# Kernel optimization log

Hardware: AMD Instinct MI355X
Metric: run time of the kernel (lower is better)

Reference implementation:

```python
import jax, jax.numpy as jnp
import numpy as np

# Config mirrors cfg['cluster'] and point_cloud_range from init_kwargs
PCR = np.array([-51.2, -51.2, -5.0, 51.2, 51.2, 3.0], dtype=np.float32)
VOXEL_SIZE = 0.2
SIZE_X = 512  # floor((51.2 - (-51.2)) / 0.2)
EPS = 1.5
MIN_SAMPLES = 5
MIN_P_CLUSTER = 20


def _cluster(points):
    """Faithful jax version of Cluster.forward for batch_size == 1.

    voxel_down_sample -> DBSCAN (euclidean, eps, min_samples) on voxel coords
    -> drop clusters with < MIN_P_CLUSTER voxels -> scatter labels back to points.
    """
    N = points.shape[0]
    # --- voxel_down_sample ---
    coords = jnp.floor((points[:, 1:3] - PCR[:2]) / VOXEL_SIZE).astype(jnp.int32)  # (N,2) x,y
    merged = coords[:, 1] * SIZE_X + coords[:, 0]
    # static-size unique: padded entries get fill_value=-1 at the end
    uniq, inv = jnp.unique(merged, size=N, fill_value=-1, return_inverse=True)
    valid = uniq >= 0  # (N,) real voxels
    vox = jnp.stack([uniq % SIZE_X, uniq // SIZE_X], axis=1).astype(jnp.float32)  # (N,2)

    # --- DBSCAN on voxel coords ---
    d2 = jnp.sum((vox[:, None, :] - vox[None, :, :]) ** 2, axis=-1)  # (N,N)
    adj = (d2 <= EPS * EPS) & valid[:, None] & valid[None, :]  # includes self-edge
    core = (jnp.sum(adj, axis=1) >= MIN_SAMPLES) & valid  # sklearn counts self

    BIG = N  # sentinel > any label
    labels0 = jnp.where(core, jnp.arange(N), BIG)
    adj_core = adj & core[None, :]

    def min_core_neighbor(labels):
        return jnp.min(jnp.where(adj_core, labels[None, :], BIG), axis=1)

    def body(carry):
        labels, _ = carry
        new = jnp.where(core, jnp.minimum(labels, min_core_neighbor(labels)), labels)
        return new, jnp.any(new != labels)

    # min-label propagation = connected components over core-core eps graph
    labels, _ = jax.lax.while_loop(lambda c: c[1], body, (labels0, jnp.array(True)))

    # border points attach to a neighboring core cluster; otherwise noise (-1)
    nb = min_core_neighbor(labels)
    raw = jnp.where(core, labels, jnp.where(valid & (nb < BIG), nb, -1))  # root-id or -1

    # relabel root-ids to consecutive 0..k-1 (sklearn numbering by smallest core idx)
    roots = jnp.unique(raw, size=N, fill_value=BIG)  # sorted; BIG padding at end
    pos = jnp.searchsorted(roots, raw)
    dense = pos - (roots[0] == -1).astype(pos.dtype)
    dense = jnp.where(raw >= 0, dense, -1)

    # drop small clusters (by voxel count), keep remaining ids unchanged
    counts = jnp.zeros(N, jnp.int32).at[jnp.where(dense >= 0, dense, 0)].add(
        jnp.where(dense >= 0, 1, 0))
    keep = counts >= MIN_P_CLUSTER
    final = jnp.where((dense >= 0) & keep[jnp.clip(dense, 0, N - 1)], dense, -1)

    # scatter voxel labels back to points (points_inst_idx has points.dtype, like torch)
    pts_inst = final[inv].astype(points.dtype)
    max_num_inst = jnp.maximum(jnp.max(final) + 1, 0)
    return pts_inst, max_num_inst


def setup_inputs() -> dict:
    key = jax.random.key(0)
    N = 8192
    k1, k2, k3, k4, k5, k6, k7 = jax.random.split(key, 7)
    n_blobs = 64
    centers = jax.random.uniform(k1, (n_blobs, 2), minval=-48.0, maxval=48.0)
    assign = jax.random.randint(k2, (N,), 0, n_blobs)
    xy = centers[assign] + jax.random.normal(k3, (N, 2)) * 1.0
    noise = jax.random.uniform(k4, (N,)) < 0.2
    xy = jnp.where(noise[:, None], jax.random.uniform(k5, (N, 2), minval=-51.0, maxval=51.0), xy)
    xy = jnp.clip(xy, -51.0, 51.0)
    z = jax.random.uniform(k6, (N, 1), minval=-3.0, maxval=1.0)
    feat = jax.random.normal(k7, (N, 1))
    points = jnp.concatenate([jnp.zeros((N, 1)), xy, z, feat], axis=1).astype(jnp.float32)
    return {"points": points, "batch_size": 1}


def reference(points, batch_size):
    # voxel_down_sample asserts batch_size == 1; single-batch path.
    return _cluster(points)
```

## Files before the change

kernel.cpp:

```cpp
#include <hip/hip_runtime.h>
#include <stdint.h>


#define GRIDW 512
#define WPR 16
#define NWORDS 8192
#define NCELLS 262144
#define NONE 0xFFFFFFFFu

#define OFF_OCC    0
#define OFF_ROOTBM 8192
#define OFF_CM     16384
#define OFF_LAB    24576
#define OFF_CNT    286720
#define FILL_BYTES (NWORDS * 4)

__device__ __forceinline__ void hsum(uint32_t l, uint32_t c, uint32_t r,
                                     uint32_t& h0, uint32_t& h1) {
  uint32_t Wb = (c << 1) | (l >> 31);
  uint32_t Eb = (c >> 1) | (r << 31);
  h0 = Wb ^ c ^ Eb;
  h1 = (Wb & c) | (Eb & (Wb ^ c));
}

__device__ __forceinline__ uint32_t ge5(uint32_t a0, uint32_t a1, uint32_t b0,
                                        uint32_t b1, uint32_t c0, uint32_t c1) {
  uint32_t u0 = a0 ^ b0, cy = a0 & b0;
  uint32_t t = a1 ^ b1;
  uint32_t u1 = t ^ cy;
  uint32_t u2 = (a1 & b1) | (cy & t);
  uint32_t v0 = u0 ^ c0, k0 = u0 & c0;
  uint32_t t2 = u1 ^ c1;
  uint32_t v1 = t2 ^ k0;
  uint32_t k1 = (u1 & c1) | (k0 & t2);
  uint32_t v2 = u2 ^ k1;
  uint32_t v3 = u2 & k1;
  return v3 | (v2 & (v1 | v0));
}

__device__ __forceinline__ uint32_t aread(uint32_t* p) {
  return __hip_atomic_load(p, __ATOMIC_RELAXED, __HIP_MEMORY_SCOPE_AGENT);
}

__device__ __forceinline__ uint32_t findc(uint32_t* L, uint32_t x) {
  uint32_t r = x, p = aread(&L[r]);
  while (p != r) { r = p; p = aread(&L[r]); }
  while (x > r) {
    uint32_t nx = aread(&L[x]);
    if (nx <= r) break;
    atomicCAS(&L[x], nx, r);
    x = nx;
  }
  return r;
}

__device__ __forceinline__ void unite(uint32_t* L, uint32_t a, uint32_t b) {
  for (;;) {
    a = findc(L, a);
    b = findc(L, b);
    if (a == b) return;
    uint32_t lo = min(a, b), hi = max(a, b);
    if (atomicCAS(&L[hi], hi, lo) == hi) return;
    a = lo; b = hi;
  }
}

__global__ void k_vox(const float* __restrict__ pts, uint32_t* __restrict__ ws,
                      int npts) {
  int i = blockIdx.x * 256 + threadIdx.x;
  if (i >= npts) return;
  float x = pts[i * 5 + 1];
  float y = pts[i * 5 + 2];
  int cx = (int)floorf((x - (-51.2f)) / 0.2f);
  int cy = (int)floorf((y - (-51.2f)) / 0.2f);
  cx = min(max(cx, 0), GRIDW - 1);
  cy = min(max(cy, 0), GRIDW - 1);
  int cell = cy * GRIDW + cx;
  uint32_t old = atomicOr(&ws[OFF_OCC + (cell >> 5)], 1u << (cell & 31));
  if (!((old >> (cell & 31)) & 1)) {
    ws[OFF_LAB + cell] = (uint32_t)cell;
    ws[OFF_CNT + cell] = 0u;
  }
}

__global__ void k_cm(uint32_t* __restrict__ ws) {
  int wi = blockIdx.x * 256 + threadIdx.x;
  const uint32_t* occ = ws + OFF_OCC;
  ws[OFF_ROOTBM + wi] = 0u;
  uint32_t cB = occ[wi];
  int y = wi >> 4, wx = wi & 15;
  uint32_t lB = wx ? occ[wi - 1] : 0u;
  uint32_t rB = (wx < 15) ? occ[wi + 1] : 0u;
  uint32_t cA = 0, lA = 0, rA = 0, cC = 0, lC = 0, rC = 0;
  if (y > 0) { int w = wi - WPR; cA = occ[w]; lA = wx ? occ[w - 1] : 0u; rA = (wx < 15) ? occ[w + 1] : 0u; }
  if (y < GRIDW - 1) { int w = wi + WPR; cC = occ[w]; lC = wx ? occ[w - 1] : 0u; rC = (wx < 15) ? occ[w + 1] : 0u; }
  uint32_t a0, a1, b0, b1, c0, c1;
  hsum(lA, cA, rA, a0, a1); hsum(lB, cB, rB, b0, b1); hsum(lC, cC, rC, c0, c1);
  ws[OFF_CM + wi] = ge5(a0, a1, b0, b1, c0, c1) & cB;
}

__global__ void k_merge(uint32_t* __restrict__ ws) {
  int cell = blockIdx.x * 256 + threadIdx.x;
  const uint32_t* cm = ws + OFF_CM;
  uint32_t* lab = ws + OFF_LAB;
  int wi = cell >> 5, b = cell & 31, wx = wi & 15, y = cell >> 9;
  uint32_t cw0 = cm[wi];
  if (!((cw0 >> b) & 1)) return;
  bool eC = (b < 31) ? (((cw0 >> (b + 1)) & 1) != 0)
                     : ((wx < 15) ? ((cm[wi + 1] & 1u) != 0) : false);
  if (eC) unite(lab, cell, cell + 1);
  if (y < GRIDW - 1) {
    uint32_t cmS = cm[wi + WPR];
    if ((cmS >> b) & 1) unite(lab, cell, cell + GRIDW);
    bool seC = (b < 31) ? (((cmS >> (b + 1)) & 1) != 0)
                        : ((wx < 15) ? ((cm[wi + WPR + 1] & 1u) != 0) : false);
    if (seC) unite(lab, cell, cell + GRIDW + 1);
    bool swC = (b > 0) ? (((cmS >> (b - 1)) & 1) != 0)
                       : ((wx > 0) ? ((cm[wi + WPR - 1] >> 31) != 0) : false);
    if (swC) unite(lab, cell, cell + GRIDW - 1);
  }
}

__global__ void k_cb(uint32_t* __restrict__ ws) {
  int cell = blockIdx.x * 256 + threadIdx.x;
  const uint32_t* occ = ws + OFF_OCC;
  const uint32_t* cm = ws + OFF_CM;
  uint32_t* lab = ws + OFF_LAB;
  uint32_t* cnt = ws + OFF_CNT;
  int wi = cell >> 5, b = cell & 31, wx = wi & 15, y = cell >> 9;
  if (!((occ[wi] >> b) & 1)) return;
  uint32_t cw0 = cm[wi];
  if ((cw0 >> b) & 1) {
    uint32_t root = findc(lab, cell);
    lab[cell] = root;
    if (root == (uint32_t)cell) atomicOr(&ws[OFF_ROOTBM + wi], 1u << b);
    atomicAdd(&cnt[root], 1u);
  } else {
    uint32_t m = NONE;
    bool t;
    t = (b > 0) ? (((cw0 >> (b - 1)) & 1) != 0)
                : ((wx > 0) ? ((cm[wi - 1] >> 31) != 0) : false);
    if (t) m = min(m, findc(lab, cell - 1));
    t = (b < 31) ? (((cw0 >> (b + 1)) & 1) != 0)
                 : ((wx < 15) ? ((cm[wi + 1] & 1u) != 0) : false);
    if (t) m = min(m, findc(lab, cell + 1));
    if (y > 0) {
      uint32_t cmN = cm[wi - WPR];
      if ((cmN >> b) & 1) m = min(m, findc(lab, cell - GRIDW));
      t = (b > 0) ? (((cmN >> (b - 1)) & 1) != 0)
                  : ((wx > 0) ? ((cm[wi - WPR - 1] >> 31) != 0) : false);
      if (t) m = min(m, findc(lab, cell - GRIDW - 1));
      t = (b < 31) ? (((cmN >> (b + 1)) & 1) != 0)
                   : ((wx < 15) ? ((cm[wi - WPR + 1] & 1u) != 0) : false);
      if (t) m = min(m, findc(lab, cell - GRIDW + 1));
    }
    if (y < GRIDW - 1) {
      uint32_t cmS = cm[wi + WPR];
      if ((cmS >> b) & 1) m = min(m, findc(lab, cell + GRIDW));
      t = (b > 0) ? (((cmS >> (b - 1)) & 1) != 0)
                  : ((wx > 0) ? ((cm[wi + WPR - 1] >> 31) != 0) : false);
      if (t) m = min(m, findc(lab, cell + GRIDW - 1));
      t = (b < 31) ? (((cmS >> (b + 1)) & 1) != 0)
                   : ((wx < 15) ? ((cm[wi + WPR + 1] & 1u) != 0) : false);
      if (t) m = min(m, findc(lab, cell + GRIDW + 1));
    }
    lab[cell] = m;
    if (m != NONE) atomicAdd(&cnt[m], 1u);
  }
}

__global__ __launch_bounds__(256) void k_scatter(
    const float* __restrict__ pts, uint32_t* __restrict__ ws,
    float* __restrict__ out, int npts) {
  __shared__ uint32_t rpre_s[NWORDS];
  __shared__ uint32_t keep_s[NWORDS];
  __shared__ uint32_t wsum[4];
  __shared__ int smax;
  int tid = threadIdx.x;
  if (tid == 0) smax = -1;
  int base = tid * 32;
  uint32_t s = 0;
  for (int j = 0; j < 32; j++) s += __popc(ws[OFF_ROOTBM + base + j]);
  int lane = tid & 63, wv = tid >> 6;
  uint32_t inc = s;
  for (int d = 1; d < 64; d <<= 1) { uint32_t t = __shfl_up(inc, d); if (lane >= d) inc += t; }
  if (lane == 63) wsum[wv] = inc;
  __syncthreads();
  uint32_t woff = 0;
  for (int k = 0; k < wv; k++) woff += wsum[k];
  uint32_t excl = woff + inc - s;
  int mx = -1;
  for (int j = 0; j < 32; j++) {
    uint32_t rbw = ws[OFF_ROOTBM + base + j];
    rpre_s[base + j] = excl;
    uint32_t rb = rbw, keep = 0;
    int d = (int)excl;
    while (rb) {
      int b2 = __ffs(rb) - 1; rb &= rb - 1;
      int r = (base + j) * 32 + b2;
      if (ws[OFF_CNT + r] >= 20u) { keep |= 1u << b2; mx = d; }
      d++;
    }
    keep_s[base + j] = keep;
    excl += __popc(rbw);
  }
  if (mx >= 0) atomicMax(&smax, mx);
  __syncthreads();
  int i = blockIdx.x * 256 + tid;
  if (i < npts) {
    float x = pts[i * 5 + 1];
    float y = pts[i * 5 + 2];
    int cx = (int)floorf((x - (-51.2f)) / 0.2f);
    int cy = (int)floorf((y - (-51.2f)) / 0.2f);
    cx = min(max(cx, 0), GRIDW - 1);
    cy = min(max(cy, 0), GRIDW - 1);
    int cell = cy * GRIDW + cx;
    uint32_t l = ws[OFF_LAB + cell];
    float o = -1.0f;
    if (l != NONE && ((keep_s[l >> 5] >> (l & 31)) & 1)) {
      int dnum = rpre_s[l >> 5] +
                 __popc(ws[OFF_ROOTBM + (l >> 5)] & ((1u << (l & 31)) - 1u));
      o = (float)dnum;
    }
    out[i] = o;
  }
  if (tid == 0) out[npts] = (float)(smax + 1);
}

extern "C" void kernel_launch(void* const* d_in, const int* in_sizes, int n_in,
                              void* d_out, int out_size, void* d_ws, size_t ws_size,
                              hipStream_t stream) {
  const float* pts = (const float*)d_in[0];
  int npts = in_sizes[0] / 5;
  uint32_t* ws = (uint32_t*)d_ws;
  float* out = (float*)d_out;
  int pblocks = (npts + 255) / 256;
  hipMemsetAsync(d_ws, 0, FILL_BYTES, stream);
  k_vox<<<pblocks, 256, 0, stream>>>(pts, ws, npts);
  k_cm<<<NWORDS / 256, 256, 0, stream>>>(ws);
  k_merge<<<NCELLS / 256, 256, 0, stream>>>(ws);
  k_cb<<<NCELLS / 256, 256, 0, stream>>>(ws);
  k_scatter<<<pblocks, 256, 0, stream>>>(pts, ws, out, npts);
}
```

Baseline: 104.3 us.

## Compact occupied and core words into worklists for merge and border kernels

k_cm now appends the indices of non-empty occupancy words and non-empty core-mask words to two compacted worklists using atomic counters. k_merge and k_cb launch 8 threads per listed word, each handling a 4-bit nibble, instead of one thread per grid cell, so threads no longer spin over the mostly empty 512x512 grid. k_vox also stores each point's cell index so k_scatter reads it back instead of recomputing it from the point coordinates. The cost is extra atomics and indirection, and the launch grids stay sized for the full word count, so many threads still exit early.

```diff
diff --git a/kernel.cpp b/kernel.cpp
--- a/kernel.cpp
+++ b/kernel.cpp
@@ -5,15 +5,19 @@
 #define GRIDW 512
 #define WPR 16
 #define NWORDS 8192
-#define NCELLS 262144
 #define NONE 0xFFFFFFFFu
 
 #define OFF_OCC    0
-#define OFF_ROOTBM 8192
-#define OFF_CM     16384
-#define OFF_LAB    24576
-#define OFF_CNT    286720
-#define FILL_BYTES (NWORDS * 4)
+#define OFF_NWM    8192
+#define OFF_NWO    8193
+#define FILL_BYTES (8194 * 4)
+#define OFF_ROOTBM 8448
+#define OFF_CM     16640
+#define OFF_PCELL  24832
+#define OFF_WLM    33024
+#define OFF_WLO    41216
+#define OFF_LAB    49408
+#define OFF_CNT    311552
 
 __device__ __forceinline__ void hsum(uint32_t l, uint32_t c, uint32_t r,
                                      uint32_t& h0, uint32_t& h1) {
@@ -76,6 +80,7 @@
   cx = min(max(cx, 0), GRIDW - 1);
   cy = min(max(cy, 0), GRIDW - 1);
   int cell = cy * GRIDW + cx;
+  ws[OFF_PCELL + i] = (uint32_t)cell;
   uint32_t old = atomicOr(&ws[OFF_OCC + (cell >> 5)], 1u << (cell & 31));
   if (!((old >> (cell & 31)) & 1)) {
     ws[OFF_LAB + cell] = (uint32_t)cell;
@@ -88,90 +93,119 @@
   const uint32_t* occ = ws + OFF_OCC;
   ws[OFF_ROOTBM + wi] = 0u;
   uint32_t cB = occ[wi];
-  int y = wi >> 4, wx = wi & 15;
-  uint32_t lB = wx ? occ[wi - 1] : 0u;
-  uint32_t rB = (wx < 15) ? occ[wi + 1] : 0u;
-  uint32_t cA = 0, lA = 0, rA = 0, cC = 0, lC = 0, rC = 0;
-  if (y > 0) { int w = wi - WPR; cA = occ[w]; lA = wx ? occ[w - 1] : 0u; rA = (wx < 15) ? occ[w + 1] : 0u; }
-  if (y < GRIDW - 1) { int w = wi + WPR; cC = occ[w]; lC = wx ? occ[w - 1] : 0u; rC = (wx < 15) ? occ[w + 1] : 0u; }
-  uint32_t a0, a1, b0, b1, c0, c1;
-  hsum(lA, cA, rA, a0, a1); hsum(lB, cB, rB, b0, b1); hsum(lC, cC, rC, c0, c1);
-  ws[OFF_CM + wi] = ge5(a0, a1, b0, b1, c0, c1) & cB;
+  uint32_t cmv = 0u;
+  if (cB) {
+    int y = wi >> 4, wx = wi & 15;
+    uint32_t lB = wx ? occ[wi - 1] : 0u;
+    uint32_t rB = (wx < 15) ? occ[wi + 1] : 0u;
+    uint32_t cA = 0, lA = 0, rA = 0, cC = 0, lC = 0, rC = 0;
+    if (y > 0) { int w = wi - WPR; cA = occ[w]; lA = wx ? occ[w - 1] : 0u; rA = (wx < 15) ? occ[w + 1] : 0u; }
+    if (y < GRIDW - 1) { int w = wi + WPR; cC = occ[w]; lC = wx ? occ[w - 1] : 0u; rC = (wx < 15) ? occ[w + 1] : 0u; }
+    uint32_t a0, a1, b0, b1, c0, c1;
+    hsum(lA, cA, rA, a0, a1); hsum(lB, cB, rB, b0, b1); hsum(lC, cC, rC, c0, c1);
+    cmv = ge5(a0, a1, b0, b1, c0, c1) & cB;
+    uint32_t io = atomicAdd(&ws[OFF_NWO], 1u);
+    ws[OFF_WLO + io] = (uint32_t)wi;
+  }
+  ws[OFF_CM + wi] = cmv;
+  if (cmv) {
+    uint32_t im = atomicAdd(&ws[OFF_NWM], 1u);
+    ws[OFF_WLM + im] = (uint32_t)wi;
+  }
 }
 
 __global__ void k_merge(uint32_t* __restrict__ ws) {
-  int cell = blockIdx.x * 256 + threadIdx.x;
+  int gid = blockIdx.x * 256 + threadIdx.x;
+  int slot = gid >> 3, nib = gid & 7;
+  if (slot >= (int)ws[OFF_NWM]) return;
+  int wi = (int)ws[OFF_WLM + slot];
   const uint32_t* cm = ws + OFF_CM;
   uint32_t* lab = ws + OFF_LAB;
-  int wi = cell >> 5, b = cell & 31, wx = wi & 15, y = cell >> 9;
   uint32_t cw0 = cm[wi];
-  if (!((cw0 >> b) & 1)) return;
-  bool eC = (b < 31) ? (((cw0 >> (b + 1)) & 1) != 0)
-                     : ((wx < 15) ? ((cm[wi + 1] & 1u) != 0) : false);
-  if (eC) unite(lab, cell, cell + 1);
-  if (y < GRIDW - 1) {
-    uint32_t cmS = cm[wi + WPR];
-    if ((cmS >> b) & 1) unite(lab, cell, cell + GRIDW);
-    bool seC = (b < 31) ? (((cmS >> (b + 1)) & 1) != 0)
-                        : ((wx < 15) ? ((cm[wi + WPR + 1] & 1u) != 0) : false);
-    if (seC) unite(lab, cell, cell + GRIDW + 1);
-    bool swC = (b > 0) ? (((cmS >> (b - 1)) & 1) != 0)
-                       : ((wx > 0) ? ((cm[wi + WPR - 1] >> 31) != 0) : false);
-    if (swC) unite(lab, cell, cell + GRIDW - 1);
+  uint32_t nmask = (cw0 >> (nib << 2)) & 0xFu;
+  if (!nmask) return;
+  int wx = wi & 15, y = wi >> 4;
+  bool hasS = y < GRIDW - 1;
+  uint32_t cmS = hasS ? cm[wi + WPR] : 0u;
+  for (int j = 0; j < 4; j++) {
+    int b = (nib << 2) + j;
+    if (!((cw0 >> b) & 1)) continue;
+    int cell = (wi << 5) + b;
+    bool eC = (b < 31) ? (((cw0 >> (b + 1)) & 1) != 0)
+                       : ((wx < 15) ? ((cm[wi + 1] & 1u) != 0) : false);
+    if (eC) unite(lab, cell, cell + 1);
+    if (hasS) {
+      if ((cmS >> b) & 1) unite(lab, cell, cell + GRIDW);
+      bool seC = (b < 31) ? (((cmS >> (b + 1)) & 1) != 0)
+                          : ((wx < 15) ? ((cm[wi + WPR + 1] & 1u) != 0) : false);
+      if (seC) unite(lab, cell, cell + GRIDW + 1);
+      bool swC = (b > 0) ? (((cmS >> (b - 1)) & 1) != 0)
+                         : ((wx > 0) ? ((cm[wi + WPR - 1] >> 31) != 0) : false);
+      if (swC) unite(lab, cell, cell + GRIDW - 1);
+    }
   }
 }
 
 __global__ void k_cb(uint32_t* __restrict__ ws) {
-  int cell = blockIdx.x * 256 + threadIdx.x;
-  const uint32_t* occ = ws + OFF_OCC;
+  int gid = blockIdx.x * 256 + threadIdx.x;
+  int slot = gid >> 3, nib = gid & 7;
+  if (slot >= (int)ws[OFF_NWO]) return;
+  int wi = (int)ws[OFF_WLO + slot];
   const uint32_t* cm = ws + OFF_CM;
   uint32_t* lab = ws + OFF_LAB;
   uint32_t* cnt = ws + OFF_CNT;
-  int wi = cell >> 5, b = cell & 31, wx = wi & 15, y = cell >> 9;
-  if (!((occ[wi] >> b) & 1)) return;
+  uint32_t oB = ws[OFF_OCC + wi];
+  uint32_t nmask = (oB >> (nib << 2)) & 0xFu;
+  if (!nmask) return;
   uint32_t cw0 = cm[wi];
-  if ((cw0 >> b) & 1) {
-    uint32_t root = findc(lab, cell);
-    lab[cell] = root;
-    if (root == (uint32_t)cell) atomicOr(&ws[OFF_ROOTBM + wi], 1u << b);
-    atomicAdd(&cnt[root], 1u);
-  } else {
-    uint32_t m = NONE;
-    bool t;
-    t = (b > 0) ? (((cw0 >> (b - 1)) & 1) != 0)
-                : ((wx > 0) ? ((cm[wi - 1] >> 31) != 0) : false);
-    if (t) m = min(m, findc(lab, cell - 1));
-    t = (b < 31) ? (((cw0 >> (b + 1)) & 1) != 0)
-                 : ((wx < 15) ? ((cm[wi + 1] & 1u) != 0) : false);
-    if (t) m = min(m, findc(lab, cell + 1));
-    if (y > 0) {
-      uint32_t cmN = cm[wi - WPR];
-      if ((cmN >> b) & 1) m = min(m, findc(lab, cell - GRIDW));
-      t = (b > 0) ? (((cmN >> (b - 1)) & 1) != 0)
-                  : ((wx > 0) ? ((cm[wi - WPR - 1] >> 31) != 0) : false);
-      if (t) m = min(m, findc(lab, cell - GRIDW - 1));
-      t = (b < 31) ? (((cmN >> (b + 1)) & 1) != 0)
-                   : ((wx < 15) ? ((cm[wi - WPR + 1] & 1u) != 0) : false);
-      if (t) m = min(m, findc(lab, cell - GRIDW + 1));
-    }
-    if (y < GRIDW - 1) {
-      uint32_t cmS = cm[wi + WPR];
-      if ((cmS >> b) & 1) m = min(m, findc(lab, cell + GRIDW));
-      t = (b > 0) ? (((cmS >> (b - 1)) & 1) != 0)
-                  : ((wx > 0) ? ((cm[wi + WPR - 1] >> 31) != 0) : false);
-      if (t) m = min(m, findc(lab, cell + GRIDW - 1));
-      t = (b < 31) ? (((cmS >> (b + 1)) & 1) != 0)
-                   : ((wx < 15) ? ((cm[wi + WPR + 1] & 1u) != 0) : false);
-      if (t) m = min(m, findc(lab, cell + GRIDW + 1));
-    }
-    lab[cell] = m;
-    if (m != NONE) atomicAdd(&cnt[m], 1u);
+  int wx = wi & 15, y = wi >> 4;
+  bool hasN = y > 0, hasS = y < GRIDW - 1;
+  uint32_t cmN = hasN ? cm[wi - WPR] : 0u;
+  uint32_t cmS = hasS ? cm[wi + WPR] : 0u;
+  for (int j = 0; j < 4; j++) {
+    int b = (nib << 2) + j;
+    if (!((oB >> b) & 1)) continue;
+    int cell = (wi << 5) + b;
+    if ((cw0 >> b) & 1) {
+      uint32_t root = findc(lab, cell);
+      lab[cell] = root;
+      if (root == (uint32_t)cell) atomicOr(&ws[OFF_ROOTBM + wi], 1u << b);
+      atomicAdd(&cnt[root], 1u);
+    } else {
+      uint32_t m = NONE;
+      bool t;
+      t = (b > 0) ? (((cw0 >> (b - 1)) & 1) != 0)
+                  : ((wx > 0) ? ((cm[wi - 1] >> 31) != 0) : false);
+      if (t) m = min(m, findc(lab, cell - 1));
+      t = (b < 31) ? (((cw0 >> (b + 1)) & 1) != 0)
+                   : ((wx < 15) ? ((cm[wi + 1] & 1u) != 0) : false);
+      if (t) m = min(m, findc(lab, cell + 1));
+      if (hasN) {
+        if ((cmN >> b) & 1) m = min(m, findc(lab, cell - GRIDW));
+        t = (b > 0) ? (((cmN >> (b - 1)) & 1) != 0)
+                    : ((wx > 0) ? ((cm[wi - WPR - 1] >> 31) != 0) : false);
+        if (t) m = min(m, findc(lab, cell - GRIDW - 1));
+        t = (b < 31) ? (((cmN >> (b + 1)) & 1) != 0)
+                     : ((wx < 15) ? ((cm[wi - WPR + 1] & 1u) != 0) : false);
+        if (t) m = min(m, findc(lab, cell - GRIDW + 1));
+      }
+      if (hasS) {
+        if ((cmS >> b) & 1) m = min(m, findc(lab, cell + GRIDW));
+        t = (b > 0) ? (((cmS >> (b - 1)) & 1) != 0)
+                    : ((wx > 0) ? ((cm[wi + WPR - 1] >> 31) != 0) : false);
+        if (t) m = min(m, findc(lab, cell + GRIDW - 1));
+        t = (b < 31) ? (((cmS >> (b + 1)) & 1) != 0)
+                     : ((wx < 15) ? ((cm[wi + WPR + 1] & 1u) != 0) : false);
+        if (t) m = min(m, findc(lab, cell + GRIDW + 1));
+      }
+      lab[cell] = m;
+      if (m != NONE) atomicAdd(&cnt[m], 1u);
+    }
   }
 }
 
 __global__ __launch_bounds__(256) void k_scatter(
-    const float* __restrict__ pts, uint32_t* __restrict__ ws,
-    float* __restrict__ out, int npts) {
+    uint32_t* __restrict__ ws, float* __restrict__ out, int npts) {
   __shared__ uint32_t rpre_s[NWORDS];
   __shared__ uint32_t keep_s[NWORDS];
   __shared__ uint32_t wsum[4];
@@ -208,13 +242,7 @@
   __syncthreads();
   int i = blockIdx.x * 256 + tid;
   if (i < npts) {
-    float x = pts[i * 5 + 1];
-    float y = pts[i * 5 + 2];
-    int cx = (int)floorf((x - (-51.2f)) / 0.2f);
-    int cy = (int)floorf((y - (-51.2f)) / 0.2f);
-    cx = min(max(cx, 0), GRIDW - 1);
-    cy = min(max(cy, 0), GRIDW - 1);
-    int cell = cy * GRIDW + cx;
+    uint32_t cell = ws[OFF_PCELL + i];
     uint32_t l = ws[OFF_LAB + cell];
     float o = -1.0f;
     if (l != NONE && ((keep_s[l >> 5] >> (l & 31)) & 1)) {
@@ -238,7 +266,7 @@
   hipMemsetAsync(d_ws, 0, FILL_BYTES, stream);
   k_vox<<<pblocks, 256, 0, stream>>>(pts, ws, npts);
   k_cm<<<NWORDS / 256, 256, 0, stream>>>(ws);
-  k_merge<<<NCELLS / 256, 256, 0, stream>>>(ws);
-  k_cb<<<NCELLS / 256, 256, 0, stream>>>(ws);
-  k_scatter<<<pblocks, 256, 0, stream>>>(pts, ws, out, npts);
-}
+  k_merge<<<NWORDS * 8 / 256, 256, 0, stream>>>(ws);
+  k_cb<<<NWORDS * 8 / 256, 256, 0, stream>>>(ws);
+  k_scatter<<<pblocks, 256, 0, stream>>>(ws, out, npts);
+}
```

Result: slower. 136.8 us (+31.2%).
